# Performance work log

Hardware: AMD Instinct MI355X
Metric: run time of the kernel (lower is better)

## Reference

```python
import jax, jax.numpy as jnp
import numpy as np

D_MODEL = 1024
NUM_HEADS = 16
SEQ_LEN = 2048
HEAD_DIM = D_MODEL // NUM_HEADS


def _rope_thetas(seq_len, head_dim):
    # Standard RoPE angles: theta[s, j] = s * 10000^(-2j/d), j in [0, d/2)
    d_half = head_dim // 2
    pos = jnp.arange(seq_len, dtype=jnp.float32)
    freqs = 1.0 / jnp.power(10000.0, jnp.arange(0, head_dim, 2, dtype=jnp.float32) / head_dim)
    thetas = pos[:, None] * freqs[None, :]  # [S, d_half]
    return jnp.cos(thetas), jnp.sin(thetas)


def _apply_rope(x, cos, sin):
    # x: [B, H, S, D]; rotate consecutive pairs (x_{2i}, x_{2i+1}) by theta_i
    b, h, s, d = x.shape
    xp = x.reshape(b, h, s, d // 2, 2)
    x1, x2 = xp[..., 0], xp[..., 1]
    c = cos[None, None, :, :]
    sn = sin[None, None, :, :]
    o1 = x1 * c - x2 * sn
    o2 = x1 * sn + x2 * c
    return jnp.stack([o1, o2], axis=-1).reshape(b, h, s, d)


def setup_inputs() -> dict:
    key = jax.random.key(0)
    k_x, k_wqkv, k_bqkv, k_wo, k_bo = jax.random.split(key, 5)
    lim_qkv = 1.0 / np.sqrt(D_MODEL)
    x = jax.random.normal(k_x, (2, SEQ_LEN, D_MODEL), dtype=jnp.float32)
    w_qkv = jax.random.uniform(k_wqkv, (3 * D_MODEL, D_MODEL), jnp.float32, -lim_qkv, lim_qkv)
    b_qkv = jax.random.uniform(k_bqkv, (3 * D_MODEL,), jnp.float32, -lim_qkv, lim_qkv)
    w_out = jax.random.uniform(k_wo, (D_MODEL, D_MODEL), jnp.float32, -lim_qkv, lim_qkv)
    b_out = jax.random.uniform(k_bo, (D_MODEL,), jnp.float32, -lim_qkv, lim_qkv)
    return {"x": x, "w_qkv": w_qkv, "b_qkv": b_qkv, "w_out": w_out, "b_out": b_out}


def reference(x, w_qkv, b_qkv, w_out, b_out):
    B, S, D = x.shape
    H, Dh = NUM_HEADS, D // NUM_HEADS
    qkv = x @ w_qkv.T + b_qkv  # [B, S, 3D]
    q, k, v = jnp.split(qkv, 3, axis=-1)
    # [B, S, D] -> [B, H, S, Dh]
    q = q.reshape(B, S, H, Dh).transpose(0, 2, 1, 3)
    k = k.reshape(B, S, H, Dh).transpose(0, 2, 1, 3)
    v = v.reshape(B, S, H, Dh).transpose(0, 2, 1, 3)
    cos, sin = _rope_thetas(S, Dh)
    q = _apply_rope(q, cos, sin)
    k = _apply_rope(k, cos, sin)
    scores = jnp.einsum('bhqd,bhkd->bhqk', q, k) / jnp.sqrt(jnp.float32(Dh))
    causal = jnp.tril(jnp.ones((S, S), dtype=bool))
    scores = jnp.where(causal[None, None, :, :], scores, jnp.float32(-jnp.inf))
    attn = jax.nn.softmax(scores, axis=-1)
    o = jnp.einsum('bhqk,bhkd->bhqd', attn, v)  # [B, H, S, Dh]
    o = o.transpose(0, 2, 1, 3).reshape(B, S, D)
    return o @ w_out.T + b_out
```

## Files before the change

### kernel.cpp

```cpp
#include <hip/hip_runtime.h>
#include <stdint.h>

#define S_LEN 2048
#define NH 16
#define DM 1024
#define HD 64
#define NB 2
#define TOK (NB * S_LEN)

typedef __attribute__((ext_vector_type(8))) short short8v;
typedef __attribute__((ext_vector_type(4))) float f32x4;
typedef __attribute__((ext_vector_type(2))) unsigned int u32x2;
typedef unsigned short u16;
typedef unsigned int u32;

__device__ __forceinline__ float bf2f(u16 u) {
    u32 x = ((u32)u) << 16;
    return __builtin_bit_cast(float, x);
}
__device__ __forceinline__ u16 f2bf(float f) {
    u32 u = __builtin_bit_cast(u32, f);
    return (u16)((u + 0x7FFFu + ((u >> 16) & 1u)) >> 16);
}
__device__ __forceinline__ u32 cvtpk(float lo, float hi) {
    u32 r;
    asm("v_cvt_pk_bf16_f32 %0, %1, %2" : "=v"(r) : "v"(lo), "v"(hi));
    return r;
}

__device__ __forceinline__ void gld_lds16(const void* g, void* lds_base_uniform) {
    auto gp = (const __attribute__((address_space(1))) u32*)(uintptr_t)g;
    auto lp = (__attribute__((address_space(3))) u32*)(uintptr_t)(u32)(uintptr_t)lds_base_uniform;
    __builtin_amdgcn_global_load_lds(gp, lp, 16, 0, 0);
}

__global__ void detect_dtype(const u32* __restrict__ xw, int* __restrict__ flag) {
    __shared__ int cnt[4];
    const int t = threadIdx.x;
    int c = 0;
#pragma unroll
    for (int j = 0; j < 16; ++j) {
        const u32 wd = xw[(t * 16 + j) * 64];
        const u32 e = (wd >> 7) & 0xFF;
        c += (e >= 0x58 && e <= 0x98) ? 1 : 0;
    }
#pragma unroll
    for (int off = 1; off < 64; off <<= 1) c += __shfl_xor(c, off);
    if ((t & 63) == 0) cnt[t >> 6] = c;
    __syncthreads();
    if (t == 0) flag[0] = (cnt[0] + cnt[1] + cnt[2] + cnt[3] >= 2600) ? 1 : 0;
}

#define XCH (TOK * DM / 8)
#define WQCH (3 * DM * DM / 8)
#define WOCH (DM * DM / 8)
__global__ __launch_bounds__(256) void convert_all(
    const void* __restrict__ xs, const void* __restrict__ wqs, const void* __restrict__ wos,
    u16* __restrict__ xd, u16* __restrict__ wqd, u16* __restrict__ wod,
    const int* __restrict__ flagp) {
    int i = blockIdx.x * 256 + threadIdx.x;
    const void* src;
    u16* dst;
    if (i < XCH) {
        src = xs; dst = xd;
    } else if (i < XCH + WQCH) {
        src = wqs; dst = wqd; i -= XCH;
    } else {
        src = wos; dst = wod; i -= XCH + WQCH;
    }
    if (flagp[0]) {
        ((short8v*)dst)[i] = ((const short8v*)src)[i];
    } else {
        const f32x4 v0 = ((const f32x4*)src)[2 * i];
        const f32x4 v1 = ((const f32x4*)src)[2 * i + 1];
        short8v o;
#pragma unroll
        for (int q = 0; q < 4; ++q) o[q] = (short)f2bf(v0[q]);
#pragma unroll
        for (int q = 0; q < 4; ++q) o[4 + q] = (short)f2bf(v1[q]);
        ((short8v*)dst)[i] = o;
    }
}

__global__ __launch_bounds__(256) void gemm_bt_bias(
    const u16* __restrict__ A, const u16* __restrict__ Bt,
    const void* __restrict__ biasv, void* __restrict__ Cv,
    int M, int N, int K, const int* __restrict__ flagp, int out_flagged) {
    __shared__ __align__(16) u16 lA[2][128 * 32];
    __shared__ __align__(16) u16 lB[2][128 * 32];
    const int fl = flagp[0];
    const int fo = out_flagged ? fl : 1;

    const int tid = threadIdx.x;
    const int w = __builtin_amdgcn_readfirstlane(tid >> 6);
    const int lane = tid & 63;
    const int quad = lane >> 4;
    const int l16 = lane & 15;
    const int bm = blockIdx.y * 128;
    const int bn = blockIdx.x * 128;
    const int wm = (w >> 1) * 64;
    const int wn = (w & 1) * 64;

    f32x4 acc[4][4];
#pragma unroll
    for (int i = 0; i < 4; ++i)
#pragma unroll
        for (int j = 0; j < 4; ++j) acc[i][j] = {0.f, 0.f, 0.f, 0.f};

    const int kiters = K >> 5;
#define GEMM_STAGE(kk, buf)                                                            \
    {                                                                                  \
        _Pragma("unroll") for (int c = 0; c < 2; ++c) {                                \
            const int chunk = w * 2 + c;                                               \
            const int off = chunk * 1024 + lane * 16;                                  \
            const int m = off >> 6;                                                    \
            const int kb_ = off & 63;                                                  \
            gld_lds16((const char*)(A + (size_t)(bm + m) * K + (kk) * 32) + kb_,       \
                      (char*)&lA[buf][0] + chunk * 1024);                              \
            gld_lds16((const char*)(Bt + (size_t)(bn + m) * K + (kk) * 32) + kb_,      \
                      (char*)&lB[buf][0] + chunk * 1024);                              \
        }                                                                              \
    }

    GEMM_STAGE(0, 0);
    int cur = 0;
    for (int kk = 0; kk < kiters; ++kk) {
        __syncthreads();
        if (kk + 1 < kiters) GEMM_STAGE(kk + 1, cur ^ 1);

        short8v af[4], bf[4];
#pragma unroll
        for (int t = 0; t < 4; ++t) {
            af[t] = *(const short8v*)&lA[cur][(wm + t * 16 + l16) * 32 + quad * 8];
            bf[t] = *(const short8v*)&lB[cur][(wn + t * 16 + l16) * 32 + quad * 8];
        }
#pragma unroll
        for (int i = 0; i < 4; ++i)
#pragma unroll
            for (int j = 0; j < 4; ++j)
                acc[i][j] = __builtin_amdgcn_mfma_f32_16x16x32_bf16(af[i], bf[j], acc[i][j], 0, 0, 0);
        cur ^= 1;
    }
#undef GEMM_STAGE

#pragma unroll
    for (int j = 0; j < 4; ++j) {
        const int col = bn + wn + j * 16 + l16;
        const float bv = fl ? bf2f(((const u16*)biasv)[col]) : ((const float*)biasv)[col];
#pragma unroll
        for (int i = 0; i < 4; ++i) {
            const int row0 = bm + wm + i * 16 + quad * 4;
#pragma unroll
            for (int r = 0; r < 4; ++r) {
                const float val = acc[i][j][r] + bv;
                const size_t idx = (size_t)(row0 + r) * N + col;
                if (fo) ((u16*)Cv)[idx] = f2bf(val);
                else ((float*)Cv)[idx] = val;
            }
        }
    }
}

__global__ __launch_bounds__(256) void rope_vt(
    const u16* __restrict__ qkv, u16* __restrict__ qws, u16* __restrict__ kws,
    u16* __restrict__ vTo) {
    __shared__ u16 tile[64 * 65];
    if (blockIdx.x < 8192) {
        const int idx = blockIdx.x * 256 + threadIdx.x;
        const int i = idx & 31;
        const int h = (idx >> 5) & 15;
        const int s = (idx >> 9) & 2047;
        const int b = idx >> 20;
        const u16* src = qkv + ((size_t)(b * S_LEN + s)) * (3 * DM) + h * HD + 2 * i;
        const u32 qp = *(const u32*)(src);
        const u32 kp = *(const u32*)(src + DM);
        const float q1 = bf2f((u16)qp), q2 = bf2f((u16)(qp >> 16));
        const float k1 = bf2f((u16)kp), k2 = bf2f((u16)(kp >> 16));
        const float freq = expf(-(float)(2 * i) * 0.14391156831212787f);
        const float th = (float)s * freq;
        float sn, cs;
        sincosf(th, &sn, &cs);
        const float oq1 = q1 * cs - q2 * sn, oq2 = q1 * sn + q2 * cs;
        const float ok1 = k1 * cs - k2 * sn, ok2 = k1 * sn + k2 * cs;
        const size_t dst = ((size_t)((b * NH + h) * S_LEN + s)) * HD + 2 * i;
        *(u32*)(qws + dst) = (u32)f2bf(oq1) | ((u32)f2bf(oq2) << 16);
        *(u32*)(kws + dst) = (u32)f2bf(ok1) | ((u32)f2bf(ok2) << 16);
    } else {
        const int bid = blockIdx.x - 8192;
        const int s0 = (bid & 31) * 64;
        const int h = (bid >> 5) & 15, b = bid >> 9;
        const int t = threadIdx.x;
#pragma unroll
        for (int it = 0; it < 16; ++it) {
            const int e = t + 256 * it;
            const int sl = e >> 6, d = e & 63;
            tile[sl * 65 + d] =
                qkv[((size_t)(b * S_LEN + s0 + sl)) * (3 * DM) + 2 * DM + h * HD + d];
        }
        __syncthreads();
#pragma unroll
        for (int it = 0; it < 16; ++it) {
            const int e = t + 256 * it;
            const int d = e >> 6, sl = e & 63;
            vTo[((size_t)((b * NH + h) * HD + d)) * S_LEN + s0 + sl] = tile[sl * 65 + d];
        }
    }
}

__global__ __launch_bounds__(256, 4) void attn_kernel(
    const u16* __restrict__ qws, const u16* __restrict__ kws,
    const u16* __restrict__ vT, u16* __restrict__ ows) {
    __shared__ __align__(16) u16 kl[2][64 * 64];
    __shared__ __align__(16) u16 vl[64 * 64];
    __shared__ __align__(16) u32 pl32[4][16 * 36];
    const int t = threadIdx.x;
    const int w = __builtin_amdgcn_readfirstlane(t >> 6);
    const int lane = t & 63;
    const int quad = lane >> 4;
    const int l16 = lane & 15;

    const int id = blockIdx.x;
    const int g = id & 31;
    const int qb = 31 - (id >> 5);
    const int h = g & 15, b = g >> 4;
    const int q0 = qb * 64 + w * 16;

    const size_t bh = (size_t)(b * NH + h);
    const u16* qbp = qws + bh * (size_t)S_LEN * HD;
    const u16* kb = kws + bh * (size_t)S_LEN * HD;
    const u16* vb = vT + bh * (size_t)HD * S_LEN;

    const int r0 = lane >> 3;
    const int srcc = (lane & 7) ^ r0;
    const int xorb = (l16 & 7) << 4;

    short8v qf[2];
#pragma unroll
    for (int hf = 0; hf < 2; ++hf)
        qf[hf] = *(const short8v*)(qbp + (size_t)(q0 + l16) * HD + hf * 32 + quad * 8);

    f32x4 oaccT[4];
#pragma unroll
    for (int d = 0; d < 4; ++d) oaccT[d] = {0.f, 0.f, 0.f, 0.f};
    float mrow = -__builtin_inff();
    float lrow = 0.f;

#pragma unroll
    for (int s = 0; s < 2; ++s) {
        const int row = w * 8 + s * 32 + r0;
        gld_lds16(kb + (size_t)row * HD + srcc * 8, (char*)&kl[0][0] + w * 1024 + s * 4096);
    }

    int cur = 0;
    for (int kt = 0; kt <= qb; ++kt) {
        __syncthreads();
#pragma unroll
        for (int s = 0; s < 2; ++s) {
            const int row = w * 8 + s * 32 + r0;
            gld_lds16(vb + (size_t)row * S_LEN + kt * 64 + srcc * 8,
                      (char*)&vl[0] + w * 1024 + s * 4096);
        }
        if (kt < qb) {
#pragma unroll
            for (int s = 0; s < 2; ++s) {
                const int row = w * 8 + s * 32 + r0;
                gld_lds16(kb + (size_t)((kt + 1) * 64 + row) * HD + srcc * 8,
                          (char*)&kl[cur ^ 1][0] + w * 1024 + s * 4096);
            }
        }
        const char* Kb = (const char*)&kl[cur][0];

        f32x4 s4[4];
        __builtin_amdgcn_s_setprio(1);
#pragma unroll
        for (int sub = 0; sub < 4; ++sub) {
            const int lin = (sub * 16 + l16) * 128 + quad * 16;
            const short8v k0 = *(const short8v*)(Kb + (lin ^ xorb));
            const short8v k1 = *(const short8v*)(Kb + ((lin + 64) ^ xorb));
            f32x4 a = {0.f, 0.f, 0.f, 0.f};
            a = __builtin_amdgcn_mfma_f32_16x16x32_bf16(k0, qf[0], a, 0, 0, 0);
            a = __builtin_amdgcn_mfma_f32_16x16x32_bf16(k1, qf[1], a, 0, 0, 0);
            s4[sub] = a;
        }
        __builtin_amdgcn_s_setprio(0);
        float sv[16];
#pragma unroll
        for (int sub = 0; sub < 4; ++sub)
#pragma unroll
            for (int r = 0; r < 4; ++r) sv[sub * 4 + r] = s4[sub][r] * 0.125f;
        if (kt == qb) {
            const int qloc = w * 16 + l16;
#pragma unroll
            for (int sub = 0; sub < 4; ++sub)
#pragma unroll
                for (int r = 0; r < 4; ++r)
                    if (sub * 16 + quad * 4 + r > qloc) sv[sub * 4 + r] = -__builtin_inff();
        }
        float a0 = fmaxf(sv[0], sv[1]), a1 = fmaxf(sv[2], sv[3]);
        float a2 = fmaxf(sv[4], sv[5]), a3 = fmaxf(sv[6], sv[7]);
        float a4 = fmaxf(sv[8], sv[9]), a5 = fmaxf(sv[10], sv[11]);
        float a6 = fmaxf(sv[12], sv[13]), a7 = fmaxf(sv[14], sv[15]);
        a0 = fmaxf(a0, a1); a2 = fmaxf(a2, a3);
        a4 = fmaxf(a4, a5); a6 = fmaxf(a6, a7);
        a0 = fmaxf(a0, a2); a4 = fmaxf(a4, a6);
        float mx = fmaxf(a0, a4);
        mx = fmaxf(mx, __shfl_xor(mx, 16));
        mx = fmaxf(mx, __shfl_xor(mx, 32));
        const float mnew = fmaxf(mrow, mx);
        const float alpha = __expf(mrow - mnew);
        mrow = mnew;
        float p[16];
#pragma unroll
        for (int i = 0; i < 16; ++i) p[i] = __expf(sv[i] - mnew);
        float b0 = p[0] + p[1], b1 = p[2] + p[3], b2 = p[4] + p[5], b3 = p[6] + p[7];
        float b4 = p[8] + p[9], b5 = p[10] + p[11], b6 = p[12] + p[13], b7 = p[14] + p[15];
        b0 += b1; b2 += b3; b4 += b5; b6 += b7;
        b0 += b2; b4 += b6;
        float ps = b0 + b4;
        ps += __shfl_xor(ps, 16);
        ps += __shfl_xor(ps, 32);
        lrow = lrow * alpha + ps;
#pragma unroll
        for (int d = 0; d < 4; ++d) oaccT[d] *= alpha;
        u32* prow = &pl32[w][l16 * 36];
#pragma unroll
        for (int sub = 0; sub < 4; ++sub) {
            u32x2 pw;
            pw.x = cvtpk(p[sub * 4 + 0], p[sub * 4 + 1]);
            pw.y = cvtpk(p[sub * 4 + 2], p[sub * 4 + 3]);
            *(u32x2*)&prow[sub * 8 + quad * 2] = pw;
        }
        asm volatile("s_waitcnt lgkmcnt(0)" ::: "memory");
        if (kt < qb) {
            asm volatile("s_waitcnt vmcnt(2)" ::: "memory");
        } else {
            asm volatile("s_waitcnt vmcnt(0)" ::: "memory");
        }
        __builtin_amdgcn_s_barrier();
        asm volatile("" ::: "memory");
        __builtin_amdgcn_s_setprio(1);
#pragma unroll
        for (int c2 = 0; c2 < 2; ++c2) {
            const short8v pf = *(const short8v*)&pl32[w][l16 * 36 + c2 * 16 + quad * 4];
#pragma unroll
            for (int d = 0; d < 4; ++d) {
                const int lin = (d * 16 + l16) * 128 + c2 * 64 + quad * 16;
                const short8v vfd = *(const short8v*)((const char*)&vl[0] + (lin ^ xorb));
                oaccT[d] = __builtin_amdgcn_mfma_f32_16x16x32_bf16(vfd, pf, oaccT[d], 0, 0, 0);
            }
        }
        __builtin_amdgcn_s_setprio(0);
        cur ^= 1;
    }

    const float inv = 1.0f / lrow;
    const size_t rowbase = ((size_t)(b * S_LEN + q0 + l16)) * DM + h * HD;
#pragma unroll
    for (int df = 0; df < 4; ++df) {
        const int d0 = df * 16 + quad * 4;
        u32x2 ov;
        ov.x = cvtpk(oaccT[df][0] * inv, oaccT[df][1] * inv);
        ov.y = cvtpk(oaccT[df][2] * inv, oaccT[df][3] * inv);
        *(u32x2*)(ows + rowbase + d0) = ov;
    }
}

extern "C" void kernel_launch(void* const* d_in, const int* in_sizes, int n_in,
                              void* d_out, int out_size, void* d_ws, size_t ws_size,
                              hipStream_t stream) {
    const void* x = d_in[0];
    const void* w_qkv = d_in[1];
    const void* b_qkv = d_in[2];
    const void* w_out = d_in[3];
    const void* b_out = d_in[4];

    int* flag = (int*)d_ws;
    u16* qkv = (u16*)d_ws + 8;
    u16* qws = qkv + (size_t)TOK * 3 * DM;
    u16* kws = qws + (size_t)NB * NH * S_LEN * HD;
    u16* vT = kws + (size_t)NB * NH * S_LEN * HD;
    u16* woutb = vT + (size_t)NB * NH * HD * S_LEN;
    u16* ows = qkv;
    u16* xb = qws;
    u16* wqkvb = kws;

    detect_dtype<<<1, 256, 0, stream>>>((const u32*)x, flag);
    convert_all<<<(XCH + WQCH + WOCH) / 256, 256, 0, stream>>>(
        x, w_qkv, w_out, xb, wqkvb, woutb, flag);

    gemm_bt_bias<<<dim3(3 * DM / 128, TOK / 128), 256, 0, stream>>>(
        xb, wqkvb, b_qkv, qkv, TOK, 3 * DM, DM, flag, 0);
    rope_vt<<<8192 + 1024, 256, 0, stream>>>(qkv, qws, kws, vT);
    attn_kernel<<<dim3(32 * 32), 256, 0, stream>>>(qws, kws, vT, ows);
    gemm_bt_bias<<<dim3(DM / 128, TOK / 128), 256, 0, stream>>>(
        ows, woutb, b_out, d_out, TOK, DM, DM, flag, 1);
}
```

Before: 218.3 us.

## Triple-buffer GEMM LDS pipeline with vmcnt waits and vectorized epilogue stores

Switches the bias GEMM from a double-buffered to a triple-buffered LDS prefetch. It prefetches two stages ahead and uses explicit vmcnt waits with a raw s_barrier in place of __syncthreads, so global-to-LDS loads can overlap more compute. MFMA operands are swapped so each lane holds four consecutive columns, which lets the epilogue write packed bf16x4 or f32x4 vectors and load the bias vectorized. It also raises wave priority around the MFMA block. The costs are 50% more LDS, which may cut occupancy, and the risk that the hand-written waitcnt does not match the async load count.

New measurement: 215.5 us. About the same (-1.3%).

```diff
diff --git a/kernel.cpp b/kernel.cpp
--- a/kernel.cpp
+++ b/kernel.cpp
@@ -86,8 +86,8 @@
     const u16* __restrict__ A, const u16* __restrict__ Bt,
     const void* __restrict__ biasv, void* __restrict__ Cv,
     int M, int N, int K, const int* __restrict__ flagp, int out_flagged) {
-    __shared__ __align__(16) u16 lA[2][128 * 32];
-    __shared__ __align__(16) u16 lB[2][128 * 32];
+    __shared__ __align__(16) u16 lA[3][128 * 32];
+    __shared__ __align__(16) u16 lB[3][128 * 32];
     const int fl = flagp[0];
     const int fo = out_flagged ? fl : 1;
 
@@ -113,20 +113,29 @@
         _Pragma("unroll") for (int c = 0; c < 2; ++c) {                                \
             const int chunk = w * 2 + c;                                               \
             const int off = chunk * 1024 + lane * 16;                                  \
-            const int m = off >> 6;                                                    \
+            const int m_ = off >> 6;                                                   \
             const int kb_ = off & 63;                                                  \
-            gld_lds16((const char*)(A + (size_t)(bm + m) * K + (kk) * 32) + kb_,       \
+            gld_lds16((const char*)(A + (size_t)(bm + m_) * K + (kk) * 32) + kb_,      \
                       (char*)&lA[buf][0] + chunk * 1024);                              \
-            gld_lds16((const char*)(Bt + (size_t)(bn + m) * K + (kk) * 32) + kb_,      \
+            gld_lds16((const char*)(Bt + (size_t)(bn + m_) * K + (kk) * 32) + kb_,     \
                       (char*)&lB[buf][0] + chunk * 1024);                              \
         }                                                                              \
     }
 
     GEMM_STAGE(0, 0);
+    if (kiters > 1) GEMM_STAGE(1, 1);
     int cur = 0;
     for (int kk = 0; kk < kiters; ++kk) {
-        __syncthreads();
-        if (kk + 1 < kiters) GEMM_STAGE(kk + 1, cur ^ 1);
+        if (kk + 1 < kiters) {
+            asm volatile("s_waitcnt vmcnt(4)" ::: "memory");
+        } else {
+            asm volatile("s_waitcnt vmcnt(0)" ::: "memory");
+        }
+        __builtin_amdgcn_s_barrier();
+        if (kk + 2 < kiters) {
+            const int nb = (cur + 2 >= 3) ? cur - 1 : cur + 2;
+            GEMM_STAGE(kk + 2, nb);
+        }
 
         short8v af[4], bf[4];
 #pragma unroll
@@ -134,28 +143,44 @@
             af[t] = *(const short8v*)&lA[cur][(wm + t * 16 + l16) * 32 + quad * 8];
             bf[t] = *(const short8v*)&lB[cur][(wn + t * 16 + l16) * 32 + quad * 8];
         }
+        __builtin_amdgcn_s_setprio(1);
 #pragma unroll
         for (int i = 0; i < 4; ++i)
 #pragma unroll
             for (int j = 0; j < 4; ++j)
-                acc[i][j] = __builtin_amdgcn_mfma_f32_16x16x32_bf16(af[i], bf[j], acc[i][j], 0, 0, 0);
-        cur ^= 1;
+                acc[i][j] = __builtin_amdgcn_mfma_f32_16x16x32_bf16(bf[j], af[i], acc[i][j], 0, 0, 0);
+        __builtin_amdgcn_s_setprio(0);
+        cur = (cur == 2) ? 0 : cur + 1;
     }
 #undef GEMM_STAGE
 
 #pragma unroll
     for (int j = 0; j < 4; ++j) {
-        const int col = bn + wn + j * 16 + l16;
-        const float bv = fl ? bf2f(((const u16*)biasv)[col]) : ((const float*)biasv)[col];
+        const int n0 = bn + wn + j * 16 + quad * 4;
+        float bv0, bv1, bv2, bv3;
+        if (fl) {
+            const u32x2 bw = *(const u32x2*)((const u16*)biasv + n0);
+            bv0 = bf2f((u16)(bw.x & 0xffff));
+            bv1 = bf2f((u16)(bw.x >> 16));
+            bv2 = bf2f((u16)(bw.y & 0xffff));
+            bv3 = bf2f((u16)(bw.y >> 16));
+        } else {
+            const f32x4 bw = *(const f32x4*)((const float*)biasv + n0);
+            bv0 = bw[0]; bv1 = bw[1]; bv2 = bw[2]; bv3 = bw[3];
+        }
 #pragma unroll
         for (int i = 0; i < 4; ++i) {
-            const int row0 = bm + wm + i * 16 + quad * 4;
-#pragma unroll
-            for (int r = 0; r < 4; ++r) {
-                const float val = acc[i][j][r] + bv;
-                const size_t idx = (size_t)(row0 + r) * N + col;
-                if (fo) ((u16*)Cv)[idx] = f2bf(val);
-                else ((float*)Cv)[idx] = val;
+            const size_t base = (size_t)(bm + wm + i * 16 + l16) * N + n0;
+            const float v0 = acc[i][j][0] + bv0, v1 = acc[i][j][1] + bv1;
+            const float v2 = acc[i][j][2] + bv2, v3 = acc[i][j][3] + bv3;
+            if (fo) {
+                u32x2 ov;
+                ov.x = cvtpk(v0, v1);
+                ov.y = cvtpk(v2, v3);
+                *(u32x2*)((u16*)Cv + base) = ov;
+            } else {
+                f32x4 ov = {v0, v1, v2, v3};
+                *(f32x4*)((float*)Cv + base) = ov;
             }
         }
     }
```
